# Optimization experiments

Measured on AMD Instinct MI355X. Metric: run time of the kernel, lower is better.

## Reference

```python
import jax, jax.numpy as jnp
import numpy as np
from jax import lax

B, C, H, W = 2, 64, 64, 64


def _conv1x1(x, w, b):
    # w: [Cout, Cin], x: [B, Cin, H, W]
    return jnp.einsum('oi,bihw->bohw', w, x) + b[None, :, None, None]


def _conv3x3(x, w, b):
    # w: [Cout, Cin, 3, 3]
    y = lax.conv_general_dilated(x, w, (1, 1), 'SAME',
                                 dimension_numbers=('NCHW', 'OIHW', 'NCHW'))
    return y + b[None, :, None, None]


def _bn(x, s, b, m, v, eps=1e-5):
    # eval-mode batchnorm with running stats
    inv = s / jnp.sqrt(v + eps)
    return x * inv[None, :, None, None] + (b - m * inv)[None, :, None, None]


def _prelu(x, a):
    return jnp.where(x > 0, x, a * x)


def _forward(x, g,
             pam_q_w, pam_q_b, pam_k_w, pam_k_b, pam_v_w, pam_v_b,
             pam_qg_w, pam_qg_b, pam_kg_w, pam_kg_b, gamma_p,
             se_fc1_w, se_fc2_w, gamma_c,
             pconv1_w, pconv1_b, pbn1_s, pbn1_b, pbn1_m, pbn1_v, pprelu1,
             pconv2_w, pconv2_b, pbn2_s, pbn2_b, pbn2_m, pbn2_v, pprelu2,
             cconv1_w, cconv1_b, cbn1_s, cbn1_b, cbn1_m, cbn1_v, cprelu1,
             cconv2_w, cconv2_b, cbn2_s, cbn2_b, cbn2_m, cbn2_v, cprelu2,
             fconv_w, fconv_b, fbn_s, fbn_b, fbn_m, fbn_v, fprelu):
    b, c, h, w = x.shape
    n = h * w
    sm = jax.nn.softmax
    # ---- G_PAM: position attention with guided double softmax ----
    q = _conv1x1(x, pam_q_w, pam_q_b).reshape(b, c, n)
    k = _conv1x1(x, pam_k_w, pam_k_b).reshape(b, c, n)
    v = _conv1x1(x, pam_v_w, pam_v_b).reshape(b, c, n)
    qg = _conv1x1(g, pam_qg_w, pam_qg_b).reshape(b, -1, n)
    kg = _conv1x1(g, pam_kg_w, pam_kg_b).reshape(b, -1, n)
    att = sm(jnp.einsum('bcn,bcm->bnm', q, k), axis=-1)        # [B,N,N]
    att_g = sm(jnp.einsum('bcn,bcm->bnm', qg, kg), axis=-1)    # [B,N,N]
    gatt = sm(jnp.einsum('bnk,bkm->bnm', att, att_g), axis=-1) # [B,N,N]
    pam_o = jnp.einsum('bcm,bnm->bcn', v, gatt).reshape(b, c, h, w)
    pam = gamma_p * pam_o + x
    # ---- pconv head ----
    t = _prelu(_bn(_conv3x3(pam, pconv1_w, pconv1_b), pbn1_s, pbn1_b, pbn1_m, pbn1_v), pprelu1)
    pam2 = _prelu(_bn(_conv1x1(t, pconv2_w, pconv2_b), pbn2_s, pbn2_b, pbn2_m, pbn2_v), pprelu2)
    # ---- G_CAM: channel attention with SE-gated guide ----
    xq = pam2.reshape(b, c, n)
    att_c = sm(jnp.einsum('bcn,bdn->bcd', xq, xq), axis=-1)    # [B,C,C]
    gy = g.mean((2, 3))  # SE: [B,C]
    gy = jax.nn.sigmoid(jnp.einsum('oc,bc->bo', se_fc2_w,
                                   jax.nn.relu(jnp.einsum('rc,bc->br', se_fc1_w, gy))))
    gq = (g * gy[:, :, None, None]).reshape(b, c, n)
    att_cg = sm(jnp.einsum('bcn,bdn->bcd', gq, gq), axis=-1)   # [B,C,C]
    ge = jnp.einsum('bck,bkd->bcd', att_c, att_cg)
    ge = jnp.max(ge, axis=-1, keepdims=True) - ge
    gatt_c = sm(ge, axis=-1)
    cam_o = jnp.einsum('bcd,bdn->bcn', gatt_c, xq).reshape(b, c, h, w)
    cam = gamma_c * cam_o + pam2
    # ---- cconv + fconv heads ----
    t = _prelu(_bn(_conv3x3(cam, cconv1_w, cconv1_b), cbn1_s, cbn1_b, cbn1_m, cbn1_v), cprelu1)
    cam2 = _prelu(_bn(_conv1x1(t, cconv2_w, cconv2_b), cbn2_s, cbn2_b, cbn2_m, cbn2_v), cprelu2)
    final = _prelu(_bn(_conv1x1(cam2, fconv_w, fconv_b), fbn_s, fbn_b, fbn_m, fbn_v), fprelu)
    return final


def setup_inputs() -> dict:
    key = jax.random.key(0)
    keys = iter(jax.random.split(key, 64))
    nk = lambda: next(keys)
    f32 = jnp.float32
    nrm = lambda shape, s=0.1: s * jax.random.normal(nk(), shape, f32)
    d = {}
    d['x'] = jax.random.normal(nk(), (B, C, H, W), f32)
    d['g'] = jax.random.normal(nk(), (B, C, H, W), f32)
    for p in ['pam_q', 'pam_k', 'pam_v', 'pam_qg', 'pam_kg']:
        d[p + '_w'] = nrm((C, C))
        d[p + '_b'] = nrm((C,))
    d['gamma_p'] = jnp.asarray(0.5, f32)
    d['se_fc1_w'] = nrm((C // 2, C))
    d['se_fc2_w'] = nrm((C, C // 2))
    d['gamma_c'] = jnp.asarray(0.5, f32)
    for pre in ['p', 'c']:
        d[pre + 'conv1_w'] = nrm((C, C, 3, 3), 0.05)
        d[pre + 'conv1_b'] = nrm((C,))
        d[pre + 'bn1_s'] = 1.0 + nrm((C,))
        d[pre + 'bn1_b'] = nrm((C,))
        d[pre + 'bn1_m'] = nrm((C,))
        d[pre + 'bn1_v'] = 1.0 + 0.1 * jax.random.uniform(nk(), (C,), f32)
        d[pre + 'prelu1'] = jnp.asarray(0.25, f32)
        d[pre + 'conv2_w'] = nrm((C, C))
        d[pre + 'conv2_b'] = nrm((C,))
        d[pre + 'bn2_s'] = 1.0 + nrm((C,))
        d[pre + 'bn2_b'] = nrm((C,))
        d[pre + 'bn2_m'] = nrm((C,))
        d[pre + 'bn2_v'] = 1.0 + 0.1 * jax.random.uniform(nk(), (C,), f32)
        d[pre + 'prelu2'] = jnp.asarray(0.25, f32)
    d['fconv_w'] = nrm((C, C))
    d['fconv_b'] = nrm((C,))
    d['fbn_s'] = 1.0 + nrm((C,))
    d['fbn_b'] = nrm((C,))
    d['fbn_m'] = nrm((C,))
    d['fbn_v'] = 1.0 + 0.1 * jax.random.uniform(nk(), (C,), f32)
    d['fprelu'] = jnp.asarray(0.25, f32)
    return d


def reference(x, g,
              pam_q_w, pam_q_b, pam_k_w, pam_k_b, pam_v_w, pam_v_b,
              pam_qg_w, pam_qg_b, pam_kg_w, pam_kg_b, gamma_p,
              se_fc1_w, se_fc2_w, gamma_c,
              pconv1_w, pconv1_b, pbn1_s, pbn1_b, pbn1_m, pbn1_v, pprelu1,
              pconv2_w, pconv2_b, pbn2_s, pbn2_b, pbn2_m, pbn2_v, pprelu2,
              cconv1_w, cconv1_b, cbn1_s, cbn1_b, cbn1_m, cbn1_v, cprelu1,
              cconv2_w, cconv2_b, cbn2_s, cbn2_b, cbn2_m, cbn2_v, cprelu2,
              fconv_w, fconv_b, fbn_s, fbn_b, fbn_m, fbn_v, fprelu):
    return _forward(x, g,
                    pam_q_w, pam_q_b, pam_k_w, pam_k_b, pam_v_w, pam_v_b,
                    pam_qg_w, pam_qg_b, pam_kg_w, pam_kg_b, gamma_p,
                    se_fc1_w, se_fc2_w, gamma_c,
                    pconv1_w, pconv1_b, pbn1_s, pbn1_b, pbn1_m, pbn1_v, pprelu1,
                    pconv2_w, pconv2_b, pbn2_s, pbn2_b, pbn2_m, pbn2_v, pprelu2,
                    cconv1_w, cconv1_b, cbn1_s, cbn1_b, cbn1_m, cbn1_v, cprelu1,
                    cconv2_w, cconv2_b, cbn2_s, cbn2_b, cbn2_m, cbn2_v, cprelu2,
                    fconv_w, fconv_b, fbn_s, fbn_b, fbn_m, fbn_v, fprelu)
```

## Files before the change

### kernel.cpp

```cpp
#include <hip/hip_runtime.h>
#include <hip/hip_fp8.h>


typedef float f32x4 __attribute__((ext_vector_type(4)));
typedef __bf16 bf16x8 __attribute__((ext_vector_type(8)));
typedef int int4v __attribute__((ext_vector_type(4)));
typedef int int8v __attribute__((ext_vector_type(8)));
typedef unsigned short ushort8 __attribute__((ext_vector_type(8)));
typedef unsigned char uchar8 __attribute__((ext_vector_type(8)));

#define DI __device__ __forceinline__

DI float bf2f(unsigned short u) { union { unsigned int i; float f; } x; x.i = ((unsigned int)u) << 16; return x.f; }
DI unsigned short f2bf(float f) { union { float f; unsigned int i; } x; x.f = f; unsigned int r = x.i + 0x7fff + ((x.i >> 16) & 1); return (unsigned short)(r >> 16); }
DI unsigned char f2fp8(float f) { __hip_fp8_e4m3 h(f); return (unsigned char)h.__x; }
DI float sane(float x) { return (x > -1e8f) ? ((x < 1e8f) ? x : 1e8f) : -1e8f; }

DI void async16(const unsigned short* g, unsigned short* l) {
    __builtin_amdgcn_global_load_lds(
        (const __attribute__((address_space(1))) void*)g,
        (__attribute__((address_space(3))) void*)l, 16, 0, 0);
}
DI void async16b(const unsigned char* g, unsigned char* l) {
    __builtin_amdgcn_global_load_lds(
        (const __attribute__((address_space(1))) void*)g,
        (__attribute__((address_space(3))) void*)l, 16, 0, 0);
}

__global__ __launch_bounds__(256) void diag_fill(float* __restrict__ out, int n, float val)
{
    int i = blockIdx.x * 256 + threadIdx.x;
    if (i < n) out[i] = val;
}

__global__ __launch_bounds__(256) void gemm_score(
    const unsigned short* __restrict__ A,
    const unsigned short* __restrict__ B,
    unsigned short* __restrict__ C, int N, long abStride, long cStride)
{
    A += (long)blockIdx.z * abStride;
    B += (long)blockIdx.z * abStride;
    C += (long)blockIdx.z * cStride;
    const int tid  = threadIdx.x;
    const int bm   = blockIdx.y, bn = blockIdx.x;
    const int lane = tid & 63, wid = tid >> 6;
    const int wm   = (wid >> 1) * 64, wn = (wid & 1) * 64;
    const int l16  = lane & 15, quad = lane >> 4;

    f32x4 acc[4][4] = {};
    bf16x8 af[2][4], bfr[2][4];
    #pragma unroll
    for (int w = 0; w < 2; w++) {
        #pragma unroll
        for (int i = 0; i < 4; i++)
            af[w][i]  = *(const bf16x8*)&A[(long)(bm * 128 + wm + i * 16 + l16) * 64 + w * 32 + quad * 8];
        #pragma unroll
        for (int j = 0; j < 4; j++)
            bfr[w][j] = *(const bf16x8*)&B[(long)(bn * 128 + wn + j * 16 + l16) * 64 + w * 32 + quad * 8];
    }
    #pragma unroll
    for (int w = 0; w < 2; w++)
        #pragma unroll
        for (int i = 0; i < 4; i++)
            #pragma unroll
            for (int j = 0; j < 4; j++)
                acc[i][j] = __builtin_amdgcn_mfma_f32_16x16x32_bf16(af[w][i], bfr[w][j], acc[i][j], 0, 0, 0);

    #pragma unroll
    for (int i = 0; i < 4; i++) {
        int rb = bm * 128 + wm + i * 16 + quad * 4;
        #pragma unroll
        for (int j = 0; j < 4; j++) {
            int col = bn * 128 + wn + j * 16 + l16;
            #pragma unroll
            for (int r = 0; r < 4; r++)
                C[(long)(rb + r) * N + col] = f2bf(acc[i][j][r]);
        }
    }
}

__global__ __launch_bounds__(256, 3) void gemm_nt(
    const unsigned short* __restrict__ A,
    const unsigned short* __restrict__ B,
    float* __restrict__ C,
    int M, int N, int K, long sA, long sB, long sC)
{
    A += (long)blockIdx.z * sA;
    B += (long)blockIdx.z * sB;
    C += (long)blockIdx.z * sC;
    __shared__ __align__(16) unsigned short As[128 * 32];
    __shared__ __align__(16) unsigned short Bs[128 * 32];
    const int tid  = threadIdx.x;
    const int bn   = blockIdx.x, slice = blockIdx.y;
    const int lane = tid & 63, wid = tid >> 6;
    const int wm   = (wid >> 1) * 64, wn = (wid & 1) * 64;
    const int l16  = lane & 15, quad = lane >> 4;

    f32x4 acc[4][4] = {};

    const int Kc   = K / (int)gridDim.y;
    const int kbeg = slice * Kc;
    const int nIter = Kc / 32;

    const int row0 = tid >> 2,        cp0 = tid & 3;
    const int row1 = (tid + 256) >> 2, cp1 = (tid + 256) & 3;
    int ar0 = row0; if (ar0 > M - 1) ar0 = M - 1;
    int ar1 = row1; if (ar1 > M - 1) ar1 = M - 1;
    const unsigned short* pa0 = &A[(long)ar0 * K + kbeg + ((cp0 ^ (row0 & 3)) * 8)];
    const unsigned short* pa1 = &A[(long)ar1 * K + kbeg + ((cp1 ^ (row1 & 3)) * 8)];
    const unsigned short* pb0 = &B[(long)(bn * 128 + row0) * K + kbeg + ((cp0 ^ (row0 & 3)) * 8)];
    const unsigned short* pb1 = &B[(long)(bn * 128 + row1) * K + kbeg + ((cp1 ^ (row1 & 3)) * 8)];
    unsigned short* la0 = &As[row0 * 32 + cp0 * 8];
    unsigned short* la1 = &As[row1 * 32 + cp1 * 8];
    unsigned short* lb0 = &Bs[row0 * 32 + cp0 * 8];
    unsigned short* lb1 = &Bs[row1 * 32 + cp1 * 8];

    const int sw = (quad ^ (l16 & 3)) * 8;

    for (int it = 0; it < nIter; it++) {
        __syncthreads();
        async16(pa0, la0);
        async16(pa1, la1);
        async16(pb0, lb0);
        async16(pb1, lb1);
        pa0 += 32; pa1 += 32; pb0 += 32; pb1 += 32;
        __syncthreads();
        bf16x8 af[4], bfr[4];
        #pragma unroll
        for (int i = 0; i < 4; i++) af[i]  = *(const bf16x8*)&As[(wm + i * 16 + l16) * 32 + sw];
        #pragma unroll
        for (int j = 0; j < 4; j++) bfr[j] = *(const bf16x8*)&Bs[(wn + j * 16 + l16) * 32 + sw];
        #pragma unroll
        for (int i = 0; i < 4; i++)
            #pragma unroll
            for (int j = 0; j < 4; j++)
                acc[i][j] = __builtin_amdgcn_mfma_f32_16x16x32_bf16(af[i], bfr[j], acc[i][j], 0, 0, 0);
    }

    #pragma unroll
    for (int i = 0; i < 4; i++) {
        int rb = wm + i * 16 + quad * 4;
        #pragma unroll
        for (int j = 0; j < 4; j++) {
            int col = bn * 128 + wn + j * 16 + l16;
            #pragma unroll
            for (int r = 0; r < 4; r++) {
                int row = rb + r;
                if (row < M)
                    C[(long)slice * M * N + (long)row * N + col] = acc[i][j][r];
            }
        }
    }
}

__global__ __launch_bounds__(256, 2) void gemm_p8(
    const unsigned char* __restrict__ A,
    const unsigned char* __restrict__ B,
    unsigned short* __restrict__ C, int N, int K,
    long sA, long sB, long sC)
{
    A += (long)blockIdx.z * sA;
    B += (long)blockIdx.z * sB;
    C += (long)blockIdx.z * sC;
    __shared__ __align__(16) unsigned char As[128 * 256];
    __shared__ __align__(16) unsigned char Bs[128 * 256];
    const int tid  = threadIdx.x;
    const int bm   = blockIdx.y, bn = blockIdx.x;
    const int lane = tid & 63, wid = tid >> 6;
    const int wm   = (wid >> 1) * 64, wn = (wid & 1) * 64;
    const int l16  = lane & 15, quad = lane >> 4;

    f32x4 acc[4][4] = {};

    const int srow = tid >> 4;
    const int sp   = tid & 15;
    const int cp   = sp ^ (srow & 15);
    const unsigned char* pa = &A[(long)(bm * 128 + srow) * K + cp * 16];
    const unsigned char* pb = &B[(long)(bn * 128 + srow) * K + cp * 16];
    unsigned char* la = &As[srow * 256 + sp * 16];
    unsigned char* lb = &Bs[srow * 256 + sp * 16];
    const long gstep = 16L * K;

    const int nIter = K / 256;
    for (int it = 0; it < nIter; it++) {
        __syncthreads();
        #pragma unroll
        for (int m = 0; m < 8; m++) {
            async16b(pa + m * gstep, la + m * 4096);
            async16b(pb + m * gstep, lb + m * 4096);
        }
        pa += 256; pb += 256;
        __syncthreads();
        #pragma unroll
        for (int h = 0; h < 2; h++) {
            const int c0 = h * 8 + 2 * quad;
            const int s0 = (c0 ^ (l16 & 15)) * 16;
            const int s1 = ((c0 + 1) ^ (l16 & 15)) * 16;
            int8v bfr[4];
            #pragma unroll
            for (int j = 0; j < 4; j++) {
                const unsigned char* base = &Bs[(wn + j * 16 + l16) * 256];
                int4v v0 = *(const int4v*)(base + s0);
                int4v v1 = *(const int4v*)(base + s1);
                bfr[j][0] = v0[0]; bfr[j][1] = v0[1]; bfr[j][2] = v0[2]; bfr[j][3] = v0[3];
                bfr[j][4] = v1[0]; bfr[j][5] = v1[1]; bfr[j][6] = v1[2]; bfr[j][7] = v1[3];
            }
            #pragma unroll
            for (int i = 0; i < 4; i++) {
                const unsigned char* base = &As[(wm + i * 16 + l16) * 256];
                int4v v0 = *(const int4v*)(base + s0);
                int4v v1 = *(const int4v*)(base + s1);
                int8v af;
                af[0] = v0[0]; af[1] = v0[1]; af[2] = v0[2]; af[3] = v0[3];
                af[4] = v1[0]; af[5] = v1[1]; af[6] = v1[2]; af[7] = v1[3];
                #pragma unroll
                for (int j = 0; j < 4; j++)
                    acc[i][j] = __builtin_amdgcn_mfma_scale_f32_16x16x128_f8f6f4(
                        af, bfr[j], acc[i][j],
                        0, 0, 0, 0x7f7f7f7f, 0, 0x7f7f7f7f);
            }
        }
    }

    const float ds = 1.f / 65536.f;
    #pragma unroll
    for (int i = 0; i < 4; i++) {
        int rb = bm * 128 + wm + i * 16 + quad * 4;
        #pragma unroll
        for (int j = 0; j < 4; j++) {
            int col = bn * 128 + wn + j * 16 + l16;
            #pragma unroll
            for (int r = 0; r < 4; r++)
                C[(long)(rb + r) * N + col] = f2bf(acc[i][j][r] * ds);
        }
    }
}

__global__ __launch_bounds__(256) void row_softmax(unsigned short* __restrict__ buf, long bStride)
{
    unsigned short* p = buf + (long)blockIdx.y * bStride + (long)blockIdx.x * 4096;
    const int tid = threadIdx.x, lane = tid & 63, wid = tid >> 6;
    float v[16]; float mx = -1e30f;
    #pragma unroll
    for (int t = 0; t < 16; t++) {
        float x = sane(bf2f(p[t * 256 + tid]));
        v[t] = x; mx = fmaxf(mx, x);
    }
    #pragma unroll
    for (int o = 32; o; o >>= 1) mx = fmaxf(mx, __shfl_xor(mx, o, 64));
    __shared__ float rmax[4], rsum[4];
    if (!lane) rmax[wid] = mx;
    __syncthreads();
    mx = fmaxf(fmaxf(rmax[0], rmax[1]), fmaxf(rmax[2], rmax[3]));
    float s = 0.f;
    #pragma unroll
    for (int t = 0; t < 16; t++) { v[t] = __expf(v[t] - mx); s += v[t]; }
    #pragma unroll
    for (int o = 32; o; o >>= 1) s += __shfl_xor(s, o, 64);
    if (!lane) rsum[wid] = s;
    __syncthreads();
    s = rsum[0] + rsum[1] + rsum[2] + rsum[3];
    float inv = 1.f / s;
    #pragma unroll
    for (int t = 0; t < 16; t++) p[t * 256 + tid] = f2bf(v[t] * inv);
}

__global__ __launch_bounds__(256) void row_softmax_f8(
    const unsigned short* __restrict__ in, unsigned char* __restrict__ out,
    long inStride, long outStride)
{
    const unsigned short* p = in + (long)blockIdx.y * inStride + (long)blockIdx.x * 4096;
    unsigned char* q = out + (long)blockIdx.y * outStride + (long)blockIdx.x * 4096;
    const int tid = threadIdx.x, lane = tid & 63, wid = tid >> 6;
    float v[16]; float mx = -1e30f;
    #pragma unroll
    for (int t = 0; t < 16; t++) {
        float x = sane(bf2f(p[t * 256 + tid]));
        v[t] = x; mx = fmaxf(mx, x);
    }
    #pragma unroll
    for (int o = 32; o; o >>= 1) mx = fmaxf(mx, __shfl_xor(mx, o, 64));
    __shared__ float rmax[4], rsum[4];
    if (!lane) rmax[wid] = mx;
    __syncthreads();
    mx = fmaxf(fmaxf(rmax[0], rmax[1]), fmaxf(rmax[2], rmax[3]));
    float s = 0.f;
    #pragma unroll
    for (int t = 0; t < 16; t++) { v[t] = __expf(v[t] - mx); s += v[t]; }
    #pragma unroll
    for (int o = 32; o; o >>= 1) s += __shfl_xor(s, o, 64);
    if (!lane) rsum[wid] = s;
    __syncthreads();
    s = rsum[0] + rsum[1] + rsum[2] + rsum[3];
    float inv = 256.f / s;
    #pragma unroll
    for (int t = 0; t < 16; t++) q[t * 256 + tid] = f2fp8(v[t] * inv);
}

__global__ __launch_bounds__(256) void colsm_partial(
    const unsigned short* __restrict__ buf,
    float* __restrict__ pmx, float* __restrict__ psum,
    long bufStride, long pStride)
{
    buf  += (long)blockIdx.z * bufStride;
    pmx  += (long)blockIdx.z * pStride;
    psum += (long)blockIdx.z * pStride;
    const int tid = threadIdx.x;
    const int colgrp = tid & 63, rg = tid >> 6;
    const int cbase = blockIdx.x * 512 + colgrp * 8;
    const int r0 = blockIdx.y * 128 + rg * 32;
    const unsigned short* p = buf + (long)r0 * 4096 + cbase;
    float mx[8], s[8];
    #pragma unroll
    for (int j = 0; j < 8; j++) { mx[j] = -1e30f; s[j] = 0.f; }
    for (int r = 0; r < 32; r++) {
        ushort8 v = *(const ushort8*)(p + (long)r * 4096);
        #pragma unroll
        for (int j = 0; j < 8; j++) {
            float x = sane(bf2f(v[j]));
            float nm = fmaxf(mx[j], x);
            s[j] = s[j] * __expf(mx[j] - nm) + __expf(x - nm);
            mx[j] = nm;
        }
    }
    __shared__ float smx[4][512], ssm[4][512];
    #pragma unroll
    for (int j = 0; j < 8; j++) { smx[rg][colgrp * 8 + j] = mx[j]; ssm[rg][colgrp * 8 + j] = s[j]; }
    __syncthreads();
    for (int c = tid; c < 512; c += 256) {
        float M = fmaxf(fmaxf(smx[0][c], smx[1][c]), fmaxf(smx[2][c], smx[3][c]));
        float S = 0.f;
        #pragma unroll
        for (int i = 0; i < 4; i++) S += ssm[i][c] * __expf(smx[i][c] - M);
        int col = blockIdx.x * 512 + c;
        pmx[blockIdx.y * 4096 + col] = M;
        psum[blockIdx.y * 4096 + col] = S;
    }
}

__global__ __launch_bounds__(256) void colsm_norm_f8(
    const unsigned short* __restrict__ in, unsigned char* __restrict__ out,
    const float* __restrict__ pmx, const float* __restrict__ psum,
    long inStride, long outStride, long pStride)
{
    in   += (long)blockIdx.z * inStride;
    out  += (long)blockIdx.z * outStride;
    pmx  += (long)blockIdx.z * pStride;
    psum += (long)blockIdx.z * pStride;
    const int tid = threadIdx.x;
    const int colgrp = tid & 63, rg = tid >> 6;
    const int cbase = blockIdx.x * 512 + colgrp * 8;
    const int r0 = blockIdx.y * 128 + rg * 32;
    const unsigned short* p = in + (long)r0 * 4096 + cbase;
    unsigned char* q = out + (long)r0 * 4096 + cbase;
    float M[8], inv[8];
    #pragma unroll
    for (int j = 0; j < 8; j++) M[j] = -1e30f;
    for (int ch = 0; ch < 32; ch++) {
        #pragma unroll
        for (int j = 0; j < 8; j++) M[j] = fmaxf(M[j], pmx[ch * 4096 + cbase + j]);
    }
    float S[8];
    #pragma unroll
    for (int j = 0; j < 8; j++) S[j] = 0.f;
    for (int ch = 0; ch < 32; ch++) {
        #pragma unroll
        for (int j = 0; j < 8; j++)
            S[j] += psum[ch * 4096 + cbase + j] * __expf(pmx[ch * 4096 + cbase + j] - M[j]);
    }
    #pragma unroll
    for (int j = 0; j < 8; j++) inv[j] = 256.f / S[j];
    for (int r = 0; r < 32; r++) {
        ushort8 v = *(const ushort8*)(p + (long)r * 4096);
        uchar8 o;
        #pragma unroll
        for (int j = 0; j < 8; j++) o[j] = f2fp8(__expf(sane(bf2f(v[j])) - M[j]) * inv[j]);
        *(uchar8*)(q + (long)r * 4096) = o;
    }
}

__global__ __launch_bounds__(256) void proj_x3(
    const float* __restrict__ X,
    const float* __restrict__ Wq, const float* __restrict__ bq,
    const float* __restrict__ Wk, const float* __restrict__ bk,
    const float* __restrict__ Wv, const float* __restrict__ bv,
    unsigned short* __restrict__ qT, unsigned short* __restrict__ kT,
    unsigned short* __restrict__ vC)
{
    const int b = blockIdx.y, nt = blockIdx.x, tid = threadIdx.x;
    __shared__ float Xs[64][64];
    __shared__ float Wqs[64][65];
    __shared__ float Wks[64][65];
    __shared__ float Wvs[64][64];
    __shared__ float Bq[64], Bk[64], Bv[64];
    for (int f = tid; f < 4096; f += 256) {
        int i = f >> 6, n = f & 63;
        Xs[i][n] = X[((long)b * 64 + i) * 4096 + nt * 64 + n];
        Wqs[f & 63][f >> 6] = Wq[f];
        Wks[f & 63][f >> 6] = Wk[f];
        Wvs[f >> 6][f & 63] = Wv[f];
    }
    if (tid < 64) { Bq[tid] = bq[tid]; Bk[tid] = bk[tid]; Bv[tid] = bv[tid]; }
    __syncthreads();
    const int c = tid & 63, g = tid >> 6;
    {
        float acc[16];
        #pragma unroll
        for (int j = 0; j < 16; j++) acc[j] = Bq[c];
        for (int i = 0; i < 64; i++) {
            float wv = Wqs[i][c];
            #pragma unroll
            for (int j = 0; j < 16; j++) acc[j] += wv * Xs[i][g + 4 * j];
        }
        unsigned short* ob = qT + ((long)b * 4096 + nt * 64) * 64;
        #pragma unroll
        for (int j = 0; j < 16; j++) ob[(g + 4 * j) * 64 + c] = f2bf(acc[j]);
    }
    {
        float acc[16];
        #pragma unroll
        for (int j = 0; j < 16; j++) acc[j] = Bk[c];
        for (int i = 0; i < 64; i++) {
            float wv = Wks[i][c];
            #pragma unroll
            for (int j = 0; j < 16; j++) acc[j] += wv * Xs[i][g + 4 * j];
        }
        unsigned short* ob = kT + ((long)b * 4096 + nt * 64) * 64;
        #pragma unroll
        for (int j = 0; j < 16; j++) ob[(g + 4 * j) * 64 + c] = f2bf(acc[j]);
    }
    {
        const int n = tid & 63, gg = tid >> 6;
        float acc[16];
        #pragma unroll
        for (int j = 0; j < 16; j++) acc[j] = Bv[gg + 4 * j];
        for (int i = 0; i < 64; i++) {
            float xv = Xs[i][n];
            #pragma unroll
            for (int j = 0; j < 16; j++) acc[j] += Wvs[gg + 4 * j][i] * xv;
        }
        unsigned short* ob = vC + ((long)b * 64) * 4096 + nt * 64;
        #pragma unroll
        for (int j = 0; j < 16; j++) ob[(long)(gg + 4 * j) * 4096 + n] = f2bf(acc[j]);
    }
}

__global__ __launch_bounds__(256) void proj_g2(
    const float* __restrict__ G,
    const float* __restrict__ Wq, const float* __restrict__ bq,
    const float* __restrict__ Wk, const float* __restrict__ bk,
    unsigned short* __restrict__ qgT, unsigned short* __restrict__ kgT)
{
    const int b = blockIdx.y, nt = blockIdx.x, tid = threadIdx.x;
    __shared__ float Xs[64][64];
    __shared__ float Wqs[64][65];
    __shared__ float Wks[64][65];
    __shared__ float Bq[64], Bk[64];
    for (int f = tid; f < 4096; f += 256) {
        int i = f >> 6, n = f & 63;
        Xs[i][n] = G[((long)b * 64 + i) * 4096 + nt * 64 + n];
        Wqs[f & 63][f >> 6] = Wq[f];
        Wks[f & 63][f >> 6] = Wk[f];
    }
    if (tid < 64) { Bq[tid] = bq[tid]; Bk[tid] = bk[tid]; }
    __syncthreads();
    const int c = tid & 63, g = tid >> 6;
    {
        float acc[16];
        #pragma unroll
        for (int j = 0; j < 16; j++) acc[j] = Bq[c];
        for (int i = 0; i < 64; i++) {
            float wv = Wqs[i][c];
            #pragma unroll
            for (int j = 0; j < 16; j++) acc[j] += wv * Xs[i][g + 4 * j];
        }
        unsigned short* ob = qgT + ((long)b * 4096 + nt * 64) * 64;
        #pragma unroll
        for (int j = 0; j < 16; j++) ob[(g + 4 * j) * 64 + c] = f2bf(acc[j]);
    }
    {
        float acc[16];
        #pragma unroll
        for (int j = 0; j < 16; j++) acc[j] = Bk[c];
        for (int i = 0; i < 64; i++) {
            float wv = Wks[i][c];
            #pragma unroll
            for (int j = 0; j < 16; j++) acc[j] += wv * Xs[i][g + 4 * j];
        }
        unsigned short* ob = kgT + ((long)b * 4096 + nt * 64) * 64;
        #pragma unroll
        for (int j = 0; j < 16; j++) ob[(g + 4 * j) * 64 + c] = f2bf(acc[j]);
    }
}

__global__ __launch_bounds__(256) void combine_pam(
    const float* __restrict__ part, const float* __restrict__ x,
    const float* __restrict__ gammaPtr, float* __restrict__ pam, int nsplit,
    long sPart, long sX)
{
    part += (long)blockIdx.y * sPart;
    x    += (long)blockIdx.y * sX;
    pam  += (long)blockIdx.y * sX;
    int i = blockIdx.x * 256 + threadIdx.x;
    float s = 0.f;
    for (int k = 0; k < nsplit; k++) s += part[(long)k * 262144 + i];
    pam[i] = gammaPtr[0] * s + x[i];
}

__global__ __launch_bounds__(256) void conv3x3_bn(
    const float* __restrict__ X, const float* __restrict__ W9,
    const float* __restrict__ bias,
    const float* __restrict__ bns, const float* __restrict__ bnb,
    const float* __restrict__ bnm, const float* __restrict__ bnv,
    const float* __restrict__ prelu, float* __restrict__ out)
{
    const int b = blockIdx.y, h = blockIdx.x, co0 = blockIdx.z * 16, tid = threadIdx.x;
    __shared__ float Ls[3][64][66];
    __shared__ float ep0[64], ep1[64], ep2[64];
    __shared__ float alpha;
    for (int f = tid; f < 3 * 64 * 64; f += 256) {
        int ky = f >> 12, rem = f & 4095, ci = rem >> 6, w = rem & 63;
        int hh = h + ky - 1;
        Ls[ky][ci][w + 1] = (hh >= 0 && hh < 64) ? X[(((long)b * 64 + ci) * 64 + hh) * 64 + w] : 0.f;
    }
    for (int f = tid; f < 192; f += 256) {
        int ky = f >> 6, ci = f & 63;
        Ls[ky][ci][0] = 0.f; Ls[ky][ci][65] = 0.f;
    }
    if (tid < 64) {
        float inv = bns[tid] * rsqrtf(fmaxf(bnv[tid], 0.f) + 1e-5f);
        ep0[tid] = inv; ep1[tid] = bnb[tid] - bnm[tid] * inv; ep2[tid] = bias[tid];
    }
    if (tid == 0) alpha = prelu[0];
    __syncthreads();
    const int w = tid & 63, g = tid >> 6;
    float acc[4];
    #pragma unroll
    for (int j = 0; j < 4; j++) acc[j] = ep2[co0 + g * 4 + j];
    for (int ci = 0; ci < 64; ci++) {
        float v0 = Ls[0][ci][w], v1 = Ls[0][ci][w + 1], v2 = Ls[0][ci][w + 2];
        float v3 = Ls[1][ci][w], v4 = Ls[1][ci][w + 1], v5 = Ls[1][ci][w + 2];
        float v6 = Ls[2][ci][w], v7 = Ls[2][ci][w + 1], v8 = Ls[2][ci][w + 2];
        #pragma unroll
        for (int j = 0; j < 4; j++) {
            const float* wp = &W9[((co0 + g * 4 + j) * 64 + ci) * 9];
            acc[j] += wp[0] * v0 + wp[1] * v1 + wp[2] * v2
                    + wp[3] * v3 + wp[4] * v4 + wp[5] * v5
                    + wp[6] * v6 + wp[7] * v7 + wp[8] * v8;
        }
    }
    #pragma unroll
    for (int j = 0; j < 4; j++) {
        int co = co0 + g * 4 + j;
        float y = acc[j] * ep0[co] + ep1[co];
        y = y > 0.f ? y : alpha * y;
        out[(((long)b * 64 + co) * 64 + h) * 64 + w] = y;
    }
}

__global__ __launch_bounds__(256) void conv1x1_bn(
    const float* __restrict__ X, const float* __restrict__ W,
    const float* __restrict__ bias,
    const float* __restrict__ bns, const float* __restrict__ bnb,
    const float* __restrict__ bnm, const float* __restrict__ bnv,
    const float* __restrict__ prelu, float* __restrict__ out)
{
    const int b = blockIdx.y, nt = blockIdx.x, tid = threadIdx.x;
    __shared__ float Xs[64][64];
    __shared__ float Ws[64][64];
    __shared__ float ep0[64], ep1[64], ep2[64];
    __shared__ float alpha;
    for (int f = tid; f < 4096; f += 256) {
        int i = f >> 6, n = f & 63;
        Xs[i][n] = X[((long)b * 64 + i) * 4096 + nt * 64 + n];
        Ws[f >> 6][f & 63] = W[f];
    }
    if (tid < 64) {
        float inv = bns[tid] * rsqrtf(fmaxf(bnv[tid], 0.f) + 1e-5f);
        ep0[tid] = inv; ep1[tid] = bnb[tid] - bnm[tid] * inv; ep2[tid] = bias[tid];
    }
    if (tid == 0) alpha = prelu[0];
    __syncthreads();
    const int n = tid & 63, g = tid >> 6;
    float acc[16];
    #pragma unroll
    for (int j = 0; j < 16; j++) acc[j] = ep2[g + 4 * j];
    for (int i = 0; i < 64; i++) {
        float xv = Xs[i][n];
        #pragma unroll
        for (int j = 0; j < 16; j++) acc[j] += Ws[g + 4 * j][i] * xv;
    }
    #pragma unroll
    for (int j = 0; j < 16; j++) {
        int c = g + 4 * j;
        float y = acc[j] * ep0[c] + ep1[c];
        y = y > 0.f ? y : alpha * y;
        out[((long)b * 64 + c) * 4096 + nt * 64 + n] = y;
    }
}

__global__ __launch_bounds__(256) void gram_partial(
    const float* __restrict__ X, float* __restrict__ out, float* __restrict__ gy)
{
    const int ch = blockIdx.x, b = blockIdx.y, tid = threadIdx.x;
    __shared__ float Xs[64][65];
    for (int f = tid; f < 4096; f += 256) {
        int ci = f >> 6, kk = f & 63;
        Xs[ci][kk] = X[((long)b * 64 + ci) * 4096 + ch * 64 + kk];
    }
    __syncthreads();
    const int d = tid & 63, g = tid >> 6;
    float acc[16] = {};
    for (int kk = 0; kk < 64; kk++) {
        float xd = Xs[d][kk];
        #pragma unroll
        for (int j = 0; j < 16; j++) acc[j] += Xs[g + 4 * j][kk] * xd;
    }
    #pragma unroll
    for (int j = 0; j < 16; j++)
        atomicAdd(&out[((long)b * 64 + (g + 4 * j)) * 64 + d], acc[j]);
    if (gy && tid < 64) {
        float s = 0.f;
        for (int kk = 0; kk < 64; kk++) s += Xs[tid][kk];
        atomicAdd(&gy[b * 64 + tid], s);
    }
}

__global__ __launch_bounds__(64) void cam_small(
    const float* __restrict__ gramx, const float* __restrict__ gramg,
    const float* __restrict__ gy_in, const float* __restrict__ fc1,
    const float* __restrict__ fc2, float* __restrict__ gattc)
{
    const int b = blockIdx.x, tid = threadIdx.x;
    __shared__ float Ac[64][65], Acg[64][65];
    __shared__ float gyv[64], r1[32], gys[64];
    gyv[tid] = gy_in[b * 64 + tid] * (1.f / 4096.f);
    __syncthreads();
    if (tid < 32) {
        float s = 0.f;
        for (int c = 0; c < 64; c++) s += fc1[tid * 64 + c] * gyv[c];
        r1[tid] = fmaxf(s, 0.f);
    }
    __syncthreads();
    {
        float s = 0.f;
        for (int r = 0; r < 32; r++) s += fc2[tid * 32 + r] * r1[r];
        gys[tid] = 1.f / (1.f + __expf(-sane(s)));
    }
    __syncthreads();
    {
        const float* r = gramx + ((long)b * 64 + tid) * 64;
        float mx = -1e30f;
        for (int d = 0; d < 64; d++) mx = fmaxf(mx, sane(r[d]));
        float s = 0.f;
        for (int d = 0; d < 64; d++) s += __expf(sane(r[d]) - mx);
        float inv = 1.f / s;
        for (int d = 0; d < 64; d++) Ac[tid][d] = __expf(sane(r[d]) - mx) * inv;
    }
    {
        const float* r = gramg + ((long)b * 64 + tid) * 64;
        float gc = gys[tid];
        float mx = -1e30f;
        for (int d = 0; d < 64; d++) mx = fmaxf(mx, sane(gc * gys[d] * r[d]));
        float s = 0.f;
        for (int d = 0; d < 64; d++) s += __expf(sane(gc * gys[d] * r[d]) - mx);
        float inv = 1.f / s;
        for (int d = 0; d < 64; d++) Acg[tid][d] = __expf(sane(gc * gys[d] * r[d]) - mx) * inv;
    }
    __syncthreads();
    float ge[64];
    float mx1 = -1e30f, mn = 1e30f;
    for (int d = 0; d < 64; d++) {
        float s = 0.f;
        for (int k = 0; k < 64; k++) s += Ac[tid][k] * Acg[k][d];
        ge[d] = s;
        mx1 = fmaxf(mx1, s); mn = fminf(mn, s);
    }
    float M2 = mx1 - mn;
    float s = 0.f;
    for (int d = 0; d < 64; d++) s += __expf((mx1 - ge[d]) - M2);
    float inv = 1.f / s;
    for (int d = 0; d < 64; d++)
        gattc[((long)b * 64 + tid) * 64 + d] = __expf((mx1 - ge[d]) - M2) * inv;
}

__global__ __launch_bounds__(256) void cam_apply(
    const float* __restrict__ pam2, const float* __restrict__ gattc,
    const float* __restrict__ gammaPtr, float* __restrict__ cam)
{
    const int b = blockIdx.y, nt = blockIdx.x, tid = threadIdx.x;
    __shared__ float Xs[64][64];
    __shared__ float Gt[64][64];
    for (int f = tid; f < 4096; f += 256) {
        int d = f >> 6, n = f & 63;
        Xs[d][n] = pam2[((long)b * 64 + d) * 4096 + nt * 64 + n];
        Gt[f >> 6][f & 63] = gattc[((long)b * 64 + (f >> 6)) * 64 + (f & 63)];
    }
    __syncthreads();
    const float gamma = gammaPtr[0];
    const int n = tid & 63, g = tid >> 6;
    float acc[16] = {};
    for (int d = 0; d < 64; d++) {
        float xv = Xs[d][n];
        #pragma unroll
        for (int j = 0; j < 16; j++) acc[j] += Gt[g + 4 * j][d] * xv;
    }
    #pragma unroll
    for (int j = 0; j < 16; j++) {
        int c = g + 4 * j;
        cam[((long)b * 64 + c) * 4096 + nt * 64 + n] = gamma * acc[j] + Xs[c][n];
    }
}

extern "C" void kernel_launch(void* const* d_in, const int* in_sizes, int n_in,
                              void* d_out, int out_size, void* d_ws, size_t ws_size,
                              hipStream_t stream)
{
    static const int exp_sizes[51] = {
        524288, 524288,
        4096, 64, 4096, 64, 4096, 64, 4096, 64, 4096, 64,
        1, 2048, 2048, 1,
        36864, 64, 64, 64, 64, 64, 1,
        4096, 64, 64, 64, 64, 64, 1,
        36864, 64, 64, 64, 64, 64, 1,
        4096, 64, 64, 64, 64, 64, 1,
        4096, 64, 64, 64, 64, 64, 1
    };
    bool map_ok = (n_in == 51) && (out_size == 524288);
    if (map_ok) for (int i = 0; i < 51; i++) if (in_sizes[i] != exp_sizes[i]) { map_ok = false; break; }

    const int diag_grid = (out_size + 255) / 256;
    if (!map_ok) {
        diag_fill<<<diag_grid, 256, 0, stream>>>((float*)d_out, out_size, 400.0f);
        return;
    }
    const size_t NEED_FULL = 121000000;
    if (ws_size < NEED_FULL) {
        float code = (ws_size >= 88000000) ? 100.0f : (ws_size >= 55000000 ? 200.0f : 300.0f);
        diag_fill<<<diag_grid, 256, 0, stream>>>((float*)d_out, out_size, code);
        return;
    }
    const bool big = (ws_size >= 248000000);
    const int nb = big ? 2 : 1;
    const long NN = 4096L * 4096;

    auto IN = [&](int i) { return (const float*)d_in[i]; };
    const float* X = IN(0);
    const float* G = IN(1);

    char* wp_ = (char*)d_ws;
    auto alloc = [&](size_t bytes) -> void* {
        void* p = (void*)wp_;
        wp_ += (bytes + 255) & ~(size_t)255;
        return p;
    };
    unsigned short* qT   = (unsigned short*)alloc(2L * 4096 * 64 * 2);
    unsigned short* kT   = (unsigned short*)alloc(2L * 4096 * 64 * 2);
    unsigned short* qgT  = (unsigned short*)alloc(2L * 4096 * 64 * 2);
    unsigned short* kgT  = (unsigned short*)alloc(2L * 4096 * 64 * 2);
    unsigned short* vC   = (unsigned short*)alloc(2L * 64 * 4096 * 2);
    float* part  = (float*)alloc((8L * nb) * 64 * 4096 * 4);
    float* pam   = (float*)alloc(2L * 64 * 4096 * 4);
    float* tbuf  = (float*)alloc(2L * 64 * 4096 * 4);
    float* pam2  = (float*)alloc(2L * 64 * 4096 * 4);
    float* cam   = (float*)alloc(2L * 64 * 4096 * 4);
    float* gramx = (float*)alloc(2L * 64 * 64 * 4);
    float* gramg = (float*)alloc(2L * 64 * 64 * 4);
    float* gy    = (float*)alloc(2L * 64 * 4);
    float* gattc = (float*)alloc(2L * 64 * 64 * 4);
    float* pmx   = (float*)alloc((32L * nb) * 4096 * 4);
    float* psum  = (float*)alloc((32L * nb) * 4096 * 4);
    unsigned short* pbuf   = (unsigned short*)alloc(NN * 2 * nb);
    unsigned short* attS   = (unsigned short*)alloc(NN * 2 * nb);
    unsigned char*  attF8  = (unsigned char*)alloc(NN * nb);
    unsigned char*  attgF8 = (unsigned char*)alloc(NN * nb);
    float* cam2 = tbuf;

    proj_x3<<<dim3(64, 2), 256, 0, stream>>>(X, IN(2), IN(3), IN(4), IN(5), IN(6), IN(7), qT, kT, vC);
    proj_g2<<<dim3(64, 2), 256, 0, stream>>>(G, IN(8), IN(9), IN(10), IN(11), qgT, kgT);

    const long abStr = 4096L * 64;
    const long pStr  = big ? NN : 0;
    const long pmStr = big ? 32L * 4096 : 0;
    for (int b = 0; b < 2; b += nb) {
        const unsigned short* qTb  = qT  + (long)b * abStr;
        const unsigned short* kTb  = kT  + (long)b * abStr;
        const unsigned short* qgTb = qgT + (long)b * abStr;
        const unsigned short* kgTb = kgT + (long)b * abStr;
        gemm_score<<<dim3(32, 32, nb), 256, 0, stream>>>(qTb,  kTb,  pbuf, 4096, abStr, pStr);
        gemm_score<<<dim3(32, 32, nb), 256, 0, stream>>>(kgTb, qgTb, attS, 4096, abStr, pStr);
        row_softmax_f8<<<dim3(4096, nb), 256, 0, stream>>>(pbuf, attF8, pStr, pStr);
        colsm_partial<<<dim3(8, 32, nb), 256, 0, stream>>>(attS, pmx, psum, pStr, pmStr);
        colsm_norm_f8<<<dim3(8, 32, nb), 256, 0, stream>>>(attS, attgF8, pmx, psum, pStr, pStr, pmStr);
        gemm_p8<<<dim3(32, 32, nb), 256, 0, stream>>>(attF8, attgF8, pbuf, 4096, 4096, pStr, pStr, pStr);
        row_softmax<<<dim3(4096, nb), 256, 0, stream>>>(pbuf, pStr);
        gemm_nt<<<dim3(32, 8, nb), 256, 0, stream>>>(vC + (long)b * abStr, pbuf, part,
                                                     64, 4096, 4096,
                                                     abStr, pStr, big ? 8L * 262144 : 0);
        combine_pam<<<dim3(1024, nb), 256, 0, stream>>>(part, X + (long)b * 262144, IN(12),
                                                        pam + (long)b * 262144, 8,
                                                        big ? 8L * 262144 : 0,
                                                        big ? 262144L : 0);
    }

    conv3x3_bn<<<dim3(64, 2, 4), 256, 0, stream>>>(pam, IN(16), IN(17), IN(18), IN(19), IN(20), IN(21), IN(22), tbuf);
    conv1x1_bn<<<dim3(64, 2), 256, 0, stream>>>(tbuf, IN(23), IN(24), IN(25), IN(26), IN(27), IN(28), IN(29), pam2);

    diag_fill<<<65, 256, 0, stream>>>(gramx, 16384 + 128, 0.0f);
    gram_partial<<<dim3(64, 2), 256, 0, stream>>>(pam2, gramx, nullptr);
    gram_partial<<<dim3(64, 2), 256, 0, stream>>>(G,    gramg, gy);
    cam_small<<<2, 64, 0, stream>>>(gramx, gramg, gy, IN(13), IN(14), gattc);
    cam_apply<<<dim3(64, 2), 256, 0, stream>>>(pam2, gattc, IN(15), cam);

    conv3x3_bn<<<dim3(64, 2, 4), 256, 0, stream>>>(cam, IN(30), IN(31), IN(32), IN(33), IN(34), IN(35), IN(36), pam);
    conv1x1_bn<<<dim3(64, 2), 256, 0, stream>>>(pam, IN(37), IN(38), IN(39), IN(40), IN(41), IN(42), IN(43), cam2);
    conv1x1_bn<<<dim3(64, 2), 256, 0, stream>>>(cam2, IN(44), IN(45), IN(46), IN(47), IN(48), IN(49), IN(50), (float*)d_out);
}
```

Baseline: 674.9 us.

## Split small tail kernels over output channels and fuse final two 1x1 convs

The conv1x1_bn and cam_apply kernels now split output channels across a third grid dimension (4 groups of 16), and gram_partial uses 32-pixel tiles with twice as many blocks. All three changes raise the block count from 128 to 512 or 256 so more compute units are busy. The last two 1x1 conv+BN+PReLU layers are fused into one kernel that keeps the intermediate in shared memory, which removes one launch and a full global round trip. The cost is that each channel-split block reloads the same input tile, and the tail kernels make up only a small part of total time.

```diff
diff --git a/kernel.cpp b/kernel.cpp
--- a/kernel.cpp
+++ b/kernel.cpp
@@ -565,37 +565,105 @@
     const float* __restrict__ bnm, const float* __restrict__ bnv,
     const float* __restrict__ prelu, float* __restrict__ out)
 {
-    const int b = blockIdx.y, nt = blockIdx.x, tid = threadIdx.x;
+    const int b = blockIdx.y, nt = blockIdx.x, co0 = blockIdx.z * 16, tid = threadIdx.x;
     __shared__ float Xs[64][64];
-    __shared__ float Ws[64][64];
-    __shared__ float ep0[64], ep1[64], ep2[64];
+    __shared__ float Ws[16][64];
+    __shared__ float ep0[16], ep1[16], ep2[16];
     __shared__ float alpha;
     for (int f = tid; f < 4096; f += 256) {
         int i = f >> 6, n = f & 63;
         Xs[i][n] = X[((long)b * 64 + i) * 4096 + nt * 64 + n];
-        Ws[f >> 6][f & 63] = W[f];
-    }
-    if (tid < 64) {
-        float inv = bns[tid] * rsqrtf(fmaxf(bnv[tid], 0.f) + 1e-5f);
-        ep0[tid] = inv; ep1[tid] = bnb[tid] - bnm[tid] * inv; ep2[tid] = bias[tid];
+    }
+    for (int f = tid; f < 1024; f += 256)
+        Ws[f >> 6][f & 63] = W[(co0 + (f >> 6)) * 64 + (f & 63)];
+    if (tid < 16) {
+        int c = co0 + tid;
+        float inv = bns[c] * rsqrtf(fmaxf(bnv[c], 0.f) + 1e-5f);
+        ep0[tid] = inv; ep1[tid] = bnb[c] - bnm[c] * inv; ep2[tid] = bias[c];
     }
     if (tid == 0) alpha = prelu[0];
     __syncthreads();
     const int n = tid & 63, g = tid >> 6;
-    float acc[16];
-    #pragma unroll
-    for (int j = 0; j < 16; j++) acc[j] = ep2[g + 4 * j];
+    float acc[4];
+    #pragma unroll
+    for (int j = 0; j < 4; j++) acc[j] = ep2[g * 4 + j];
     for (int i = 0; i < 64; i++) {
         float xv = Xs[i][n];
         #pragma unroll
-        for (int j = 0; j < 16; j++) acc[j] += Ws[g + 4 * j][i] * xv;
-    }
-    #pragma unroll
-    for (int j = 0; j < 16; j++) {
-        int c = g + 4 * j;
-        float y = acc[j] * ep0[c] + ep1[c];
+        for (int j = 0; j < 4; j++) acc[j] += Ws[g * 4 + j][i] * xv;
+    }
+    #pragma unroll
+    for (int j = 0; j < 4; j++) {
+        int lc = g * 4 + j;
+        float y = acc[j] * ep0[lc] + ep1[lc];
         y = y > 0.f ? y : alpha * y;
-        out[((long)b * 64 + c) * 4096 + nt * 64 + n] = y;
+        out[((long)b * 64 + co0 + lc) * 4096 + nt * 64 + n] = y;
+    }
+}
+
+__global__ __launch_bounds__(256) void conv1x1x2(
+    const float* __restrict__ X,
+    const float* __restrict__ W1, const float* __restrict__ b1,
+    const float* __restrict__ s1, const float* __restrict__ bb1,
+    const float* __restrict__ m1, const float* __restrict__ v1,
+    const float* __restrict__ p1,
+    const float* __restrict__ W2, const float* __restrict__ b2,
+    const float* __restrict__ s2, const float* __restrict__ bb2,
+    const float* __restrict__ m2, const float* __restrict__ v2,
+    const float* __restrict__ p2,
+    float* __restrict__ out)
+{
+    const int b = blockIdx.y, nt = blockIdx.x, tid = threadIdx.x;
+    __shared__ float Xs[64][33];
+    __shared__ float Y1[64][33];
+    __shared__ float W1s[64][64], W2s[64][64];
+    __shared__ float e0a[64], e1a[64], e2a[64], e0b[64], e1b[64], e2b[64];
+    __shared__ float al1, al2;
+    for (int f = tid; f < 2048; f += 256) {
+        int i = f >> 5, n = f & 31;
+        Xs[i][n] = X[((long)b * 64 + i) * 4096 + nt * 32 + n];
+    }
+    for (int f = tid; f < 4096; f += 256) {
+        W1s[f >> 6][f & 63] = W1[f];
+        W2s[f >> 6][f & 63] = W2[f];
+    }
+    if (tid < 64) {
+        float inv = s1[tid] * rsqrtf(fmaxf(v1[tid], 0.f) + 1e-5f);
+        e0a[tid] = inv; e1a[tid] = bb1[tid] - m1[tid] * inv; e2a[tid] = b1[tid];
+        inv = s2[tid] * rsqrtf(fmaxf(v2[tid], 0.f) + 1e-5f);
+        e0b[tid] = inv; e1b[tid] = bb2[tid] - m2[tid] * inv; e2b[tid] = b2[tid];
+    }
+    if (tid == 0) { al1 = p1[0]; al2 = p2[0]; }
+    __syncthreads();
+    const int n = tid & 31, g = tid >> 5;
+    float acc[8];
+    #pragma unroll
+    for (int j = 0; j < 8; j++) acc[j] = e2a[g * 8 + j];
+    for (int i = 0; i < 64; i++) {
+        float xv = Xs[i][n];
+        #pragma unroll
+        for (int j = 0; j < 8; j++) acc[j] += W1s[g * 8 + j][i] * xv;
+    }
+    #pragma unroll
+    for (int j = 0; j < 8; j++) {
+        int c = g * 8 + j;
+        float y = acc[j] * e0a[c] + e1a[c];
+        Y1[c][n] = y > 0.f ? y : al1 * y;
+    }
+    __syncthreads();
+    #pragma unroll
+    for (int j = 0; j < 8; j++) acc[j] = e2b[g * 8 + j];
+    for (int i = 0; i < 64; i++) {
+        float xv = Y1[i][n];
+        #pragma unroll
+        for (int j = 0; j < 8; j++) acc[j] += W2s[g * 8 + j][i] * xv;
+    }
+    #pragma unroll
+    for (int j = 0; j < 8; j++) {
+        int c = g * 8 + j;
+        float y = acc[j] * e0b[c] + e1b[c];
+        y = y > 0.f ? y : al2 * y;
+        out[((long)b * 64 + c) * 4096 + nt * 32 + n] = y;
     }
 }
 
@@ -603,15 +671,15 @@
     const float* __restrict__ X, float* __restrict__ out, float* __restrict__ gy)
 {
     const int ch = blockIdx.x, b = blockIdx.y, tid = threadIdx.x;
-    __shared__ float Xs[64][65];
-    for (int f = tid; f < 4096; f += 256) {
-        int ci = f >> 6, kk = f & 63;
-        Xs[ci][kk] = X[((long)b * 64 + ci) * 4096 + ch * 64 + kk];
+    __shared__ float Xs[64][33];
+    for (int f = tid; f < 2048; f += 256) {
+        int ci = f >> 5, kk = f & 31;
+        Xs[ci][kk] = X[((long)b * 64 + ci) * 4096 + ch * 32 + kk];
     }
     __syncthreads();
     const int d = tid & 63, g = tid >> 6;
     float acc[16] = {};
-    for (int kk = 0; kk < 64; kk++) {
+    for (int kk = 0; kk < 32; kk++) {
         float xd = Xs[d][kk];
         #pragma unroll
         for (int j = 0; j < 16; j++) acc[j] += Xs[g + 4 * j][kk] * xd;
@@ -621,7 +689,7 @@
         atomicAdd(&out[((long)b * 64 + (g + 4 * j)) * 64 + d], acc[j]);
     if (gy && tid < 64) {
         float s = 0.f;
-        for (int kk = 0; kk < 64; kk++) s += Xs[tid][kk];
+        for (int kk = 0; kk < 32; kk++) s += Xs[tid][kk];
         atomicAdd(&gy[b * 64 + tid], s);
     }
 }
@@ -688,26 +756,27 @@
     const float* __restrict__ pam2, const float* __restrict__ gattc,
     const float* __restrict__ gammaPtr, float* __restrict__ cam)
 {
-    const int b = blockIdx.y, nt = blockIdx.x, tid = threadIdx.x;
+    const int b = blockIdx.y, nt = blockIdx.x, co0 = blockIdx.z * 16, tid = threadIdx.x;
     __shared__ float Xs[64][64];
-    __shared__ float Gt[64][64];
+    __shared__ float Gt[16][64];
     for (int f = tid; f < 4096; f += 256) {
         int d = f >> 6, n = f & 63;
         Xs[d][n] = pam2[((long)b * 64 + d) * 4096 + nt * 64 + n];
-        Gt[f >> 6][f & 63] = gattc[((long)b * 64 + (f >> 6)) * 64 + (f & 63)];
-    }
+    }
+    for (int f = tid; f < 1024; f += 256)
+        Gt[f >> 6][f & 63] = gattc[((long)b * 64 + co0 + (f >> 6)) * 64 + (f & 63)];
     __syncthreads();
     const float gamma = gammaPtr[0];
     const int n = tid & 63, g = tid >> 6;
-    float acc[16] = {};
+    float acc[4] = {};
     for (int d = 0; d < 64; d++) {
         float xv = Xs[d][n];
         #pragma unroll
-        for (int j = 0; j < 16; j++) acc[j] += Gt[g + 4 * j][d] * xv;
-    }
-    #pragma unroll
-    for (int j = 0; j < 16; j++) {
-        int c = g + 4 * j;
+        for (int j = 0; j < 4; j++) acc[j] += Gt[g * 4 + j][d] * xv;
+    }
+    #pragma unroll
+    for (int j = 0; j < 4; j++) {
+        int c = co0 + g * 4 + j;
         cam[((long)b * 64 + c) * 4096 + nt * 64 + n] = gamma * acc[j] + Xs[c][n];
     }
 }
@@ -774,7 +843,6 @@
     unsigned short* attS   = (unsigned short*)alloc(NN * 2 * nb);
     unsigned char*  attF8  = (unsigned char*)alloc(NN * nb);
     unsigned char*  attgF8 = (unsigned char*)alloc(NN * nb);
-    float* cam2 = tbuf;
 
     proj_x3<<<dim3(64, 2), 256, 0, stream>>>(X, IN(2), IN(3), IN(4), IN(5), IN(6), IN(7), qT, kT, vC);
     proj_g2<<<dim3(64, 2), 256, 0, stream>>>(G, IN(8), IN(9), IN(10), IN(11), qgT, kgT);
@@ -804,15 +872,17 @@
     }
 
     conv3x3_bn<<<dim3(64, 2, 4), 256, 0, stream>>>(pam, IN(16), IN(17), IN(18), IN(19), IN(20), IN(21), IN(22), tbuf);
-    conv1x1_bn<<<dim3(64, 2), 256, 0, stream>>>(tbuf, IN(23), IN(24), IN(25), IN(26), IN(27), IN(28), IN(29), pam2);
+    conv1x1_bn<<<dim3(64, 2, 4), 256, 0, stream>>>(tbuf, IN(23), IN(24), IN(25), IN(26), IN(27), IN(28), IN(29), pam2);
 
     diag_fill<<<65, 256, 0, stream>>>(gramx, 16384 + 128, 0.0f);
-    gram_partial<<<dim3(64, 2), 256, 0, stream>>>(pam2, gramx, nullptr);
-    gram_partial<<<dim3(64, 2), 256, 0, stream>>>(G,    gramg, gy);
+    gram_partial<<<dim3(128, 2), 256, 0, stream>>>(pam2, gramx, nullptr);
+    gram_partial<<<dim3(128, 2), 256, 0, stream>>>(G,    gramg, gy);
     cam_small<<<2, 64, 0, stream>>>(gramx, gramg, gy, IN(13), IN(14), gattc);
-    cam_apply<<<dim3(64, 2), 256, 0, stream>>>(pam2, gattc, IN(15), cam);
+    cam_apply<<<dim3(64, 2, 4), 256, 0, stream>>>(pam2, gattc, IN(15), cam);
 
     conv3x3_bn<<<dim3(64, 2, 4), 256, 0, stream>>>(cam, IN(30), IN(31), IN(32), IN(33), IN(34), IN(35), IN(36), pam);
-    conv1x1_bn<<<dim3(64, 2), 256, 0, stream>>>(pam, IN(37), IN(38), IN(39), IN(40), IN(41), IN(42), IN(43), cam2);
-    conv1x1_bn<<<dim3(64, 2), 256, 0, stream>>>(cam2, IN(44), IN(45), IN(46), IN(47), IN(48), IN(49), IN(50), (float*)d_out);
-}
+    conv1x1x2<<<dim3(128, 2), 256, 0, stream>>>(pam,
+        IN(37), IN(38), IN(39), IN(40), IN(41), IN(42), IN(43),
+        IN(44), IN(45), IN(46), IN(47), IN(48), IN(49), IN(50),
+        (float*)d_out);
+}
```

Result: faster. 657.7 us (-2.6%).
